# Kernel tuning notes

Hardware: AMD Instinct MI355X
Metric: run time of the kernel (lower is better)

Reference implementation:

```python
import jax, jax.numpy as jnp
import numpy as np

N_NODES = 100000
N_EDGES = 3200000
F = 32          # n_node_features
L = 50          # n_node_labels
EL = 10         # n_edge_labels
K = 16          # out_dim (graph_data.num_classes)


def setup_inputs() -> dict:
    key = jax.random.key(0)
    ks = jax.random.split(key, 12)
    x = jax.random.normal(ks[0], (N_NODES, F), dtype=jnp.float32)
    node_labels = jax.random.randint(ks[1], (N_NODES,), 0, L, dtype=jnp.int32)
    edge_src = jax.random.randint(ks[2], (N_EDGES,), 0, N_NODES, dtype=jnp.int32)
    edge_dst = jax.random.randint(ks[3], (N_EDGES,), 0, N_NODES, dtype=jnp.int32)
    edge_labels = jax.random.randint(ks[4], (N_EDGES,), 0, EL, dtype=jnp.int32)
    s = 0.1
    W1 = jax.random.normal(ks[5], (L, L, EL), dtype=jnp.float32) * s
    b1 = jax.random.normal(ks[6], (L,), dtype=jnp.float32) * s
    W2 = jax.random.normal(ks[7], (L, L, EL), dtype=jnp.float32) * s
    b2 = jax.random.normal(ks[8], (L,), dtype=jnp.float32) * s
    W3 = jax.random.normal(ks[9], (L, L, EL), dtype=jnp.float32) * s
    b3 = jax.random.normal(ks[10], (L,), dtype=jnp.float32) * s
    kr1, kr2 = jax.random.split(ks[11])
    Wr = jax.random.normal(kr1, (L, F, K), dtype=jnp.float32) * s
    br = jax.random.normal(kr2, (K,), dtype=jnp.float32) * s
    return {"x": x, "W1": W1, "b1": b1, "W2": W2, "b2": b2, "W3": W3, "b3": b3,
            "Wr": Wr, "br": br, "node_labels": node_labels,
            "edge_src": edge_src, "edge_dst": edge_dst, "edge_labels": edge_labels}


def _conv(x, W, b, node_labels, edge_src, edge_dst, edge_labels):
    # weight_rule_wf: per-edge scalar weight indexed by (src label, dst label, edge label)
    w_e = W[node_labels[edge_src], node_labels[edge_dst], edge_labels]  # [E]
    msgs = w_e[:, None] * x[edge_src]                                   # [E, F]
    agg = jax.ops.segment_sum(msgs, edge_dst, num_segments=x.shape[0])  # [N, F]
    # node_label_rule bias: per-node bias indexed by node label, then Tanh
    return jnp.tanh(agg + b[node_labels][:, None])


def reference(x, W1, b1, W2, b2, W3, b3, Wr, br,
              node_labels, edge_src, edge_dst, edge_labels):
    h = _conv(x, W1, b1, node_labels, edge_src, edge_dst, edge_labels)
    h = _conv(h, W2, b2, node_labels, edge_src, edge_dst, edge_labels)
    h = _conv(h, W3, b3, node_labels, edge_src, edge_dst, edge_labels)
    # GraphResizeLayer (node_label_rule): out[k] = sum_i Wr[label_i, f, k] * h[i, f] + br[k]
    # equivalent efficient form: pre-aggregate node features by label, then contract.
    sums = jax.ops.segment_sum(h, node_labels, num_segments=Wr.shape[0])  # [L, F]
    out = jnp.tanh(jnp.einsum('lf,lfk->k', sums, Wr) + br)                # [K]
    return out
```

## Files before the change

kernel.cpp:

```cpp
#include <hip/hip_runtime.h>
#include <hip/hip_bf16.h>
#include <hip/hip_fp16.h>
#include <hip/hip_fp8.h>

#define NN 100000
#define NE 3200000
#define FF 32
#define LL 50
#define ELB 10
#define KK 16
#define NWIDX (LL * LL * ELB)

#define CH 8192
#define NBLK_P1 391
#define NBUK 391
#define CAP 9216

typedef float floatx2 __attribute__((ext_vector_type(2)));

__device__ __forceinline__ float fast_tanh(float x) {
    float e = __expf(2.0f * x);
    return 1.0f - 2.0f / (e + 1.0f);
}

__global__ __launch_bounds__(512) void p1_scatter(const int* __restrict__ esrc,
                                                  const int* __restrict__ edst,
                                                  const int* __restrict__ elab,
                                                  const float* __restrict__ x,
                                                  const float* __restrict__ W1,
                                                  const float* __restrict__ W2,
                                                  const float* __restrict__ W3,
                                                  ushort4* __restrict__ Wi,
                                                  unsigned char* __restrict__ labels8,
                                                  const int* __restrict__ labels,
                                                  unsigned* __restrict__ xb,
                                                  int* __restrict__ cursor,
                                                  unsigned* __restrict__ recs) {
    __shared__ int lcnt[NBUK];
    __shared__ int lofs[NBUK];
    __shared__ int lbase[NBUK];
    __shared__ int sc[512];
    __shared__ unsigned srec[CH];
    __shared__ unsigned sgad[CH];
    int tid = threadIdx.x;
    for (int i = blockIdx.x * 512 + tid; i < NN * FF / 4; i += NBLK_P1 * 512) {
        float4 v = ((const float4*)x)[i];
        __hip_fp8_e4m3 a(v.x), b(v.y), c(v.z), d(v.w);
        xb[i] = (unsigned)a.__x | ((unsigned)b.__x << 8) |
                ((unsigned)c.__x << 16) | ((unsigned)d.__x << 24);
    }
    for (int i = blockIdx.x * 512 + tid; i < NWIDX; i += NBLK_P1 * 512) {
        ushort4 w;
        w.x = __half_as_ushort(__float2half(W1[i]));
        w.y = __half_as_ushort(__float2half(W2[i]));
        w.z = __half_as_ushort(__float2half(W3[i]));
        w.w = 0;
        Wi[i] = w;
    }
    for (int i = blockIdx.x * 512 + tid; i < NN; i += NBLK_P1 * 512)
        labels8[i] = (unsigned char)labels[i];
    for (int i = tid; i < NBUK; i += 512) lcnt[i] = 0;
    __syncthreads();
    long e0 = (long)blockIdx.x * CH;
    long rem = NE - e0;
    int cnt = rem < CH ? (int)rem : CH;
    int nq = cnt >> 2;
    const int4* edst4 = (const int4*)(edst + e0);
    const int4* esrc4 = (const int4*)(esrc + e0);
    const int4* elab4 = (const int4*)(elab + e0);
    for (int i = tid; i < nq; i += 512) {
        int4 d = edst4[i];
        atomicAdd(&lcnt[d.x >> 8], 1);
        atomicAdd(&lcnt[d.y >> 8], 1);
        atomicAdd(&lcnt[d.z >> 8], 1);
        atomicAdd(&lcnt[d.w >> 8], 1);
    }
    __syncthreads();
    sc[tid] = (tid < NBUK) ? lcnt[tid] : 0;
    __syncthreads();
    for (int ofs = 1; ofs < 512; ofs <<= 1) {
        int t = (tid >= ofs) ? sc[tid - ofs] : 0;
        __syncthreads();
        sc[tid] += t;
        __syncthreads();
    }
    if (tid < NBUK) {
        int c = lcnt[tid];
        lofs[tid] = sc[tid] - c;
        lbase[tid] = c ? atomicAdd(&cursor[tid], c) : 0;
        lcnt[tid] = 0;
    }
    __syncthreads();
    for (int i = tid; i < nq; i += 512) {
        int4 s4 = esrc4[i];
        int4 l4 = elab4[i];
        int4 d4 = edst4[i];
#pragma unroll
        for (int k = 0; k < 4; ++k) {
            int s  = (&s4.x)[k];
            int d  = (&d4.x)[k];
            int el = (&l4.x)[k];
            int b = d >> 8;
            int pos = atomicAdd(&lcnt[b], 1);
            int slot = lofs[b] + pos;
            srec[slot] = ((unsigned)s << 12) | ((unsigned)el << 8) | (unsigned)(d & 255);
            int rel = lbase[b] + pos;
            sgad[slot] = (rel < CAP) ? (unsigned)(b * CAP + rel) : 0xFFFFFFFFu;
        }
    }
    __syncthreads();
    for (int i = tid; i < cnt; i += 512) {
        unsigned g = sgad[i];
        if (g != 0xFFFFFFFFu)
            recs[g] = srec[i];
    }
}

__global__ __launch_bounds__(512) void p2_local(const int* __restrict__ cursor,
                                                const unsigned* __restrict__ recs,
                                                const unsigned char* __restrict__ labels8,
                                                const ushort4* __restrict__ Wi,
                                                unsigned* __restrict__ ed1,
                                                unsigned* __restrict__ ed2,
                                                unsigned* __restrict__ ed3,
                                                int* __restrict__ gstart,
                                                int* __restrict__ gcnt) {
    __shared__ int deg[256], loff[256], lcur[256], sc[256];
    __shared__ int labd[256];
    __shared__ unsigned pk32[CAP];
    int b = blockIdx.x, tid = threadIdx.x;
    int base = b * CAP;
    int n = cursor[b];
    if (n > CAP) n = CAP;
    if (tid < 256) {
        int node = (b << 8) + tid;
        deg[tid] = 0;
        lcur[tid] = 0;
        labd[tid] = (node < NN) ? (int)labels8[node] : 0;
    }
    __syncthreads();
    for (int i = tid; i < n; i += 512)
        atomicAdd(&deg[(int)(recs[base + i] & 255)], 1);
    __syncthreads();
    if (tid < 256) sc[tid] = deg[tid];
    __syncthreads();
    for (int ofs = 1; ofs < 256; ofs <<= 1) {
        int t = (tid >= ofs && tid < 256) ? sc[tid - ofs] : 0;
        __syncthreads();
        if (tid < 256) sc[tid] += t;
        __syncthreads();
    }
    if (tid < 256) {
        loff[tid] = sc[tid] - deg[tid];
        int node = (b << 8) + tid;
        if (node < NN) { gstart[node] = base + loff[tid]; gcnt[node] = deg[tid]; }
    }
    __syncthreads();
    for (int i = tid; i < n; i += 512) {
        unsigned r = recs[base + i];
        int dl  = (int)(r & 255);
        int el  = (int)((r >> 8) & 15);
        int src = (int)(r >> 12);
        int widx = (int)labels8[src] * (LL * ELB) + labd[dl] * ELB + el;
        int ofs = atomicAdd(&lcur[dl], 1);
        pk32[loff[dl] + ofs] = ((unsigned)widx << 17) | (unsigned)src;
    }
    __syncthreads();
    for (int slot = tid; slot < n; slot += 512) {
        unsigned v = pk32[slot];
        int widx = (int)(v >> 17);
        unsigned sb = (v & 0x1FFFFu) << 15;
        ushort4 wv = Wi[widx];
        ed1[base + slot] = (unsigned)(wv.x >> 1) | sb;
        ed2[base + slot] = (unsigned)(wv.y >> 1) | sb;
        ed3[base + slot] = (unsigned)(wv.z >> 1) | sb;
    }
}

__global__ __launch_bounds__(256) void conv_kernel(const unsigned char* __restrict__ xin,
                                                   unsigned char* __restrict__ hout,
                                                   const int* __restrict__ gstart,
                                                   const int* __restrict__ gcnt,
                                                   const unsigned* __restrict__ ed,
                                                   const float* __restrict__ bias,
                                                   const int* __restrict__ labels) {
    __shared__ unsigned stage[2][8][64];
    int tid = threadIdx.x;
    int hw = tid >> 5, lane = tid & 31;
    int node = (blockIdx.x << 3) + hw;
    int s = gstart[node];
    int n = gcnt[node];
    float bb = bias[labels[node]];
    int eg = lane >> 3;
    int fg = (lane & 7) << 2;
    float4 acc = {0.f, 0.f, 0.f, 0.f};
    unsigned e_cur = ed[s + (lane < n ? lane : 0)];
    int buf = 0;
    for (int base = 0; base < n; base += 32) {
        int idx = base + lane;
        float w = 0.f;
        unsigned so = 0u;
        if (idx < n) {
            unsigned short h = (unsigned short)((e_cur & 0x7FFFu) << 1);
            w = __half2float(__ushort_as_half(h));
            so = (e_cur >> 15) << 5;
        }
        ((uint2*)&stage[buf][hw][0])[lane] = make_uint2(__float_as_uint(w), so);
        int nb = base + 32;
        if (nb < n) {
            int i2 = nb + lane;
            e_cur = ed[s + (i2 < n ? i2 : nb)];
        }
        __builtin_amdgcn_wave_barrier();
#pragma unroll
        for (int j = 0; j < 8; ++j) {
            uint2 ws = ((const uint2*)&stage[buf][hw][0])[j * 4 + eg];
            unsigned pv = *(const unsigned*)(xin + ws.y + fg);
            floatx2 lo = __builtin_amdgcn_cvt_pk_f32_fp8((int)pv, false);
            floatx2 hi = __builtin_amdgcn_cvt_pk_f32_fp8((int)pv, true);
            float we = __uint_as_float(ws.x);
            acc.x += we * lo.x;
            acc.y += we * lo.y;
            acc.z += we * hi.x;
            acc.w += we * hi.y;
        }
        buf ^= 1;
    }
    acc.x += __shfl_xor(acc.x, 8);  acc.y += __shfl_xor(acc.y, 8);
    acc.z += __shfl_xor(acc.z, 8);  acc.w += __shfl_xor(acc.w, 8);
    acc.x += __shfl_xor(acc.x, 16); acc.y += __shfl_xor(acc.y, 16);
    acc.z += __shfl_xor(acc.z, 16); acc.w += __shfl_xor(acc.w, 16);
    if (lane < 8) {
        __hip_fp8_e4m3 q0(fast_tanh(acc.x + bb));
        __hip_fp8_e4m3 q1(fast_tanh(acc.y + bb));
        __hip_fp8_e4m3 q2(fast_tanh(acc.z + bb));
        __hip_fp8_e4m3 q3(fast_tanh(acc.w + bb));
        unsigned pk = (unsigned)q0.__x | ((unsigned)q1.__x << 8) |
                      ((unsigned)q2.__x << 16) | ((unsigned)q3.__x << 24);
        ((unsigned*)(hout + ((long)node << 5)))[lane] = pk;
    }
}

__global__ __launch_bounds__(256) void lsum_kernel(const unsigned* __restrict__ h,
                                                   const int* __restrict__ labels,
                                                   float* __restrict__ sums) {
    __shared__ float ls[LL * FF];
    int tid = threadIdx.x;
    for (int i = tid; i < LL * FF; i += 256) ls[i] = 0.f;
    __syncthreads();
    for (int i = blockIdx.x * 256 + tid; i < NN * 8; i += gridDim.x * 256) {
        unsigned pv = h[i];
        int nodei = i >> 3;
        int fb = (i & 7) << 2;
        int l = labels[nodei];
        floatx2 lo = __builtin_amdgcn_cvt_pk_f32_fp8((int)pv, false);
        floatx2 hi = __builtin_amdgcn_cvt_pk_f32_fp8((int)pv, true);
        float* bp = &ls[l * FF + fb];
        atomicAdd(bp + 0, lo.x);
        atomicAdd(bp + 1, lo.y);
        atomicAdd(bp + 2, hi.x);
        atomicAdd(bp + 3, hi.y);
    }
    __syncthreads();
    for (int i = tid; i < LL * FF; i += 256) atomicAdd(&sums[i], ls[i]);
}

__global__ __launch_bounds__(256) void resize_kernel(const float* __restrict__ sums,
                                                     const float* __restrict__ Wr,
                                                     const float* __restrict__ br,
                                                     float* __restrict__ out) {
    __shared__ float red[256][KK];
    int tid = threadIdx.x;
    float acc[KK];
#pragma unroll
    for (int k = 0; k < KK; ++k) acc[k] = 0.f;
    for (int p = tid; p < LL * FF; p += 256) {
        float sv = sums[p];
#pragma unroll
        for (int k = 0; k < KK; ++k) acc[k] += sv * Wr[p * KK + k];
    }
#pragma unroll
    for (int k = 0; k < KK; ++k) red[tid][k] = acc[k];
    __syncthreads();
    for (int sft = 128; sft > 0; sft >>= 1) {
        if (tid < sft) {
#pragma unroll
            for (int k = 0; k < KK; ++k) red[tid][k] += red[tid + sft][k];
        }
        __syncthreads();
    }
    if (tid < KK) out[tid] = fast_tanh(red[0][tid] + br[tid]);
}

extern "C" void kernel_launch(void* const* d_in, const int* in_sizes, int n_in,
                              void* d_out, int out_size, void* d_ws, size_t ws_size,
                              hipStream_t stream) {
    const float* x   = (const float*)d_in[0];
    const float* W1  = (const float*)d_in[1];
    const float* b1  = (const float*)d_in[2];
    const float* W2  = (const float*)d_in[3];
    const float* b2  = (const float*)d_in[4];
    const float* W3  = (const float*)d_in[5];
    const float* b3  = (const float*)d_in[6];
    const float* Wr  = (const float*)d_in[7];
    const float* br  = (const float*)d_in[8];
    const int* labels = (const int*)d_in[9];
    const int* esrc   = (const int*)d_in[10];
    const int* edst   = (const int*)d_in[11];
    const int* elab   = (const int*)d_in[12];
    float* out = (float*)d_out;

    char* ws = (char*)d_ws;
    size_t o = 0;
    auto alloc = [&](size_t bytes) -> void* {
        void* p = ws + o;
        o += (bytes + 255) & ~(size_t)255;
        return p;
    };
    char* regionA = (char*)alloc((size_t)NBUK * CAP * sizeof(unsigned));
    unsigned* recs = (unsigned*)regionA;
    unsigned char* h1 = (unsigned char*)regionA;
    unsigned char* h2 = (unsigned char*)(regionA + (size_t)NN * FF);

    unsigned* ed1 = (unsigned*)alloc((size_t)NBUK * CAP * sizeof(unsigned));
    unsigned* ed2 = (unsigned*)alloc((size_t)NBUK * CAP * sizeof(unsigned));
    unsigned* ed3 = (unsigned*)alloc((size_t)NBUK * CAP * sizeof(unsigned));
    unsigned* xb = (unsigned*)alloc((size_t)NN * FF);
    ushort4* Wi  = (ushort4*)alloc((size_t)NWIDX * sizeof(ushort4));
    unsigned char* labels8 = (unsigned char*)alloc(NN);
    int* cursor = (int*)alloc(NBUK * sizeof(int));
    float* sums = (float*)alloc(LL * FF * sizeof(float));
    int* gstart = (int*)alloc(NN * sizeof(int));
    int* gcnt   = (int*)alloc(NN * sizeof(int));

    size_t msz = (size_t)((char*)sums - (char*)cursor) + LL * FF * sizeof(float);
    hipMemsetAsync(cursor, 0, msz, stream);

    p1_scatter<<<NBLK_P1, 512, 0, stream>>>(esrc, edst, elab, x, W1, W2, W3, Wi,
                                            labels8, labels, xb, cursor, recs);
    p2_local<<<NBUK, 512, 0, stream>>>(cursor, recs, labels8, Wi, ed1, ed2, ed3, gstart, gcnt);

    conv_kernel<<<NN / 8, 256, 0, stream>>>((const unsigned char*)xb, h1, gstart, gcnt, ed1, b1, labels);
    conv_kernel<<<NN / 8, 256, 0, stream>>>(h1, h2, gstart, gcnt, ed2, b2, labels);
    conv_kernel<<<NN / 8, 256, 0, stream>>>(h2, h1, gstart, gcnt, ed3, b3, labels);

    lsum_kernel<<<256, 256, 0, stream>>>((const unsigned*)h1, labels, sums);
    resize_kernel<<<1, 256, 0, stream>>>(sums, Wr, br, out);
}
```

Measured before the change: 260.9 us.

## Sort nodes by in-degree for conv load balance and trim tail iterations

Builds a degree histogram in p2_local, prefix-sums it, and scatters node ids into a degree-sorted permutation. The conv kernels then process nodes through that permutation, so the eight half-waves in a block have similar edge counts and less lane time is spent idle. The partial last chunk now runs only as many inner steps as it needs instead of a fixed eight. This adds two small kernels and an indirection, and the output writes and gathers follow the permuted order, which may hurt locality.

```diff
diff --git a/kernel.cpp b/kernel.cpp
--- a/kernel.cpp
+++ b/kernel.cpp
@@ -15,6 +15,7 @@
 #define NBLK_P1 391
 #define NBUK 391
 #define CAP 9216
+#define DBIN 128
 
 typedef float floatx2 __attribute__((ext_vector_type(2)));
 
@@ -124,9 +125,11 @@
                                                 unsigned* __restrict__ ed2,
                                                 unsigned* __restrict__ ed3,
                                                 int* __restrict__ gstart,
-                                                int* __restrict__ gcnt) {
+                                                int* __restrict__ gcnt,
+                                                int* __restrict__ hist) {
     __shared__ int deg[256], loff[256], lcur[256], sc[256];
     __shared__ int labd[256];
+    __shared__ int lh[DBIN];
     __shared__ unsigned pk32[CAP];
     int b = blockIdx.x, tid = threadIdx.x;
     int base = b * CAP;
@@ -138,6 +141,7 @@
         lcur[tid] = 0;
         labd[tid] = (node < NN) ? (int)labels8[node] : 0;
     }
+    if (tid >= 256 && tid < 256 + DBIN) lh[tid - 256] = 0;
     __syncthreads();
     for (int i = tid; i < n; i += 512)
         atomicAdd(&deg[(int)(recs[base + i] & 255)], 1);
@@ -153,9 +157,15 @@
     if (tid < 256) {
         loff[tid] = sc[tid] - deg[tid];
         int node = (b << 8) + tid;
-        if (node < NN) { gstart[node] = base + loff[tid]; gcnt[node] = deg[tid]; }
-    }
-    __syncthreads();
+        if (node < NN) {
+            gstart[node] = base + loff[tid];
+            gcnt[node] = deg[tid];
+            int d = deg[tid]; if (d > DBIN - 1) d = DBIN - 1;
+            atomicAdd(&lh[d], 1);
+        }
+    }
+    __syncthreads();
+    if (tid < DBIN && lh[tid]) atomicAdd(&hist[tid], lh[tid]);
     for (int i = tid; i < n; i += 512) {
         unsigned r = recs[base + i];
         int dl  = (int)(r & 255);
@@ -177,17 +187,44 @@
     }
 }
 
+__global__ __launch_bounds__(DBIN) void p2b_prefix(const int* __restrict__ hist,
+                                                   int* __restrict__ binoff) {
+    __shared__ int sc[DBIN];
+    int t = threadIdx.x;
+    sc[t] = hist[t];
+    __syncthreads();
+    for (int ofs = 1; ofs < DBIN; ofs <<= 1) {
+        int v = (t >= ofs) ? sc[t - ofs] : 0;
+        __syncthreads();
+        sc[t] += v;
+        __syncthreads();
+    }
+    binoff[t] = sc[t] - hist[t];
+}
+
+__global__ __launch_bounds__(256) void p3_scatter(const int* __restrict__ gcnt,
+                                                  int* __restrict__ binoff,
+                                                  int* __restrict__ perm) {
+    int node = blockIdx.x * 256 + threadIdx.x;
+    if (node < NN) {
+        int d = gcnt[node]; if (d > DBIN - 1) d = DBIN - 1;
+        int pos = atomicAdd(&binoff[d], 1);
+        perm[pos] = node;
+    }
+}
+
 __global__ __launch_bounds__(256) void conv_kernel(const unsigned char* __restrict__ xin,
                                                    unsigned char* __restrict__ hout,
                                                    const int* __restrict__ gstart,
                                                    const int* __restrict__ gcnt,
                                                    const unsigned* __restrict__ ed,
                                                    const float* __restrict__ bias,
-                                                   const int* __restrict__ labels) {
+                                                   const int* __restrict__ labels,
+                                                   const int* __restrict__ perm) {
     __shared__ unsigned stage[2][8][64];
     int tid = threadIdx.x;
     int hw = tid >> 5, lane = tid & 31;
-    int node = (blockIdx.x << 3) + hw;
+    int node = perm[(blockIdx.x << 3) + hw];
     int s = gstart[node];
     int n = gcnt[node];
     float bb = bias[labels[node]];
@@ -196,6 +233,14 @@
     float4 acc = {0.f, 0.f, 0.f, 0.f};
     unsigned e_cur = ed[s + (lane < n ? lane : 0)];
     int buf = 0;
+#define CONV_J(j) {                                                          \
+        uint2 ws = ((const uint2*)&stage[buf][hw][0])[(j) * 4 + eg];         \
+        unsigned pv = *(const unsigned*)(xin + ws.y + fg);                   \
+        floatx2 lo = __builtin_amdgcn_cvt_pk_f32_fp8((int)pv, false);        \
+        floatx2 hi = __builtin_amdgcn_cvt_pk_f32_fp8((int)pv, true);         \
+        float we = __uint_as_float(ws.x);                                    \
+        acc.x += we * lo.x;  acc.y += we * lo.y;                             \
+        acc.z += we * hi.x;  acc.w += we * hi.y; }
     for (int base = 0; base < n; base += 32) {
         int idx = base + lane;
         float w = 0.f;
@@ -212,20 +257,17 @@
             e_cur = ed[s + (i2 < n ? i2 : nb)];
         }
         __builtin_amdgcn_wave_barrier();
-#pragma unroll
-        for (int j = 0; j < 8; ++j) {
-            uint2 ws = ((const uint2*)&stage[buf][hw][0])[j * 4 + eg];
-            unsigned pv = *(const unsigned*)(xin + ws.y + fg);
-            floatx2 lo = __builtin_amdgcn_cvt_pk_f32_fp8((int)pv, false);
-            floatx2 hi = __builtin_amdgcn_cvt_pk_f32_fp8((int)pv, true);
-            float we = __uint_as_float(ws.x);
-            acc.x += we * lo.x;
-            acc.y += we * lo.y;
-            acc.z += we * hi.x;
-            acc.w += we * hi.y;
+        int L = n - base;
+        if (L >= 32) {
+            CONV_J(0) CONV_J(1) CONV_J(2) CONV_J(3)
+            CONV_J(4) CONV_J(5) CONV_J(6) CONV_J(7)
+        } else {
+            int jlim = (L + 3) >> 2;
+            for (int j = 0; j < jlim; ++j) CONV_J(j)
         }
         buf ^= 1;
     }
+#undef CONV_J
     acc.x += __shfl_xor(acc.x, 8);  acc.y += __shfl_xor(acc.y, 8);
     acc.z += __shfl_xor(acc.z, 8);  acc.w += __shfl_xor(acc.w, 8);
     acc.x += __shfl_xor(acc.x, 16); acc.y += __shfl_xor(acc.y, 16);
@@ -330,19 +372,25 @@
     unsigned char* labels8 = (unsigned char*)alloc(NN);
     int* cursor = (int*)alloc(NBUK * sizeof(int));
     float* sums = (float*)alloc(LL * FF * sizeof(float));
+    int* hist   = (int*)alloc(DBIN * sizeof(int));
+    int* binoff = (int*)alloc(DBIN * sizeof(int));
+    int* perm   = (int*)alloc(NN * sizeof(int));
     int* gstart = (int*)alloc(NN * sizeof(int));
     int* gcnt   = (int*)alloc(NN * sizeof(int));
 
-    size_t msz = (size_t)((char*)sums - (char*)cursor) + LL * FF * sizeof(float);
+    size_t msz = (size_t)((char*)hist - (char*)cursor) + DBIN * sizeof(int);
     hipMemsetAsync(cursor, 0, msz, stream);
 
     p1_scatter<<<NBLK_P1, 512, 0, stream>>>(esrc, edst, elab, x, W1, W2, W3, Wi,
                                             labels8, labels, xb, cursor, recs);
-    p2_local<<<NBUK, 512, 0, stream>>>(cursor, recs, labels8, Wi, ed1, ed2, ed3, gstart, gcnt);
-
-    conv_kernel<<<NN / 8, 256, 0, stream>>>((const unsigned char*)xb, h1, gstart, gcnt, ed1, b1, labels);
-    conv_kernel<<<NN / 8, 256, 0, stream>>>(h1, h2, gstart, gcnt, ed2, b2, labels);
-    conv_kernel<<<NN / 8, 256, 0, stream>>>(h2, h1, gstart, gcnt, ed3, b3, labels);
+    p2_local<<<NBUK, 512, 0, stream>>>(cursor, recs, labels8, Wi, ed1, ed2, ed3,
+                                       gstart, gcnt, hist);
+    p2b_prefix<<<1, DBIN, 0, stream>>>(hist, binoff);
+    p3_scatter<<<NBUK, 256, 0, stream>>>(gcnt, binoff, perm);
+
+    conv_kernel<<<NN / 8, 256, 0, stream>>>((const unsigned char*)xb, h1, gstart, gcnt, ed1, b1, labels, perm);
+    conv_kernel<<<NN / 8, 256, 0, stream>>>(h1, h2, gstart, gcnt, ed2, b2, labels, perm);
+    conv_kernel<<<NN / 8, 256, 0, stream>>>(h2, h1, gstart, gcnt, ed3, b3, labels, perm);
 
     lsum_kernel<<<256, 256, 0, stream>>>((const unsigned*)h1, labels, sums);
     resize_kernel<<<1, 256, 0, stream>>>(sums, Wr, br, out);
```

Result: slower. 460.9 us (+76.7%).
